# Optimization experiments

Measured on AMD Instinct MI355X. Metric: run time of the kernel, lower is better.

The kernel has to match this reference:

```python
import jax, jax.numpy as jnp
import numpy as np

B, T, N, D, H, M = 2, 12, 325, 64, 8, 3
EPS = 1e-6


def _layer_norm(x, g, b):
    mu = jnp.mean(x, axis=-1, keepdims=True)
    var = jnp.mean(jnp.square(x - mu), axis=-1, keepdims=True)
    return (x - mu) * jax.lax.rsqrt(var + EPS) * g + b


def _meta_w(ste, W1, b1, W2, b2):
    # ste: (b,t,n,d) -> per-token weight matrix (b,t,n,d,d)  [Meta_projection]
    h = jax.nn.relu(jnp.einsum('btnd,de->btne', ste, W1) + b1)
    w = jnp.einsum('btnd,df->btnf', h, W2) + b2
    b_, t_, n_, _ = ste.shape
    return w.reshape(b_, t_, n_, D, D)


def _meta_qkv(q, k, v, ste_q, ste_k, ste_v, mW1, mb1, mW2, mb2):
    wq = _meta_w(ste_q, mW1[0], mb1[0], mW2[0], mb2[0])
    wk = _meta_w(ste_k, mW1[1], mb1[1], mW2[1], mb2[1])
    wv = _meta_w(ste_v, mW1[2], mb1[2], mW2[2], mb2[2])
    mg = lambda x, w: jnp.einsum('btnd,btnde->btne', x, w)  # meta_guide
    return mg(q, wq), mg(k, wk), mg(v, wv)


def _split_heads(x):  # (B,L,d) -> (H*B,L,d/H), head-major = tf.concat(tf.split(x,H,-1),0)
    return jnp.concatenate(jnp.split(x, H, axis=-1), axis=0)


def _concat_heads(x):
    return jnp.concatenate(jnp.split(x, H, axis=0), axis=-1)


def _sdpa(q, k, v, tm=None):
    dk = q.shape[-1]
    scores = jnp.einsum('bqd,bkd->bqk', q, k) / jnp.sqrt(jnp.float32(dk))
    if tm is not None:  # spatial mask (n,n) broadcast over batch*heads
        scores = jnp.where(tm[None] > 0, scores, jnp.float32(-1e9))
    att = jax.nn.softmax(scores, axis=-1)
    return jnp.einsum('bqk,bkd->bqd', att, v)


def _temporal_attn(q, k, v, ste_q, ste_k, ste_v, mW1, mb1, mW2, mb2, Wo):
    b, t, n, d = q.shape
    qg, kg, vg = _meta_qkv(q, k, v, ste_q, ste_k, ste_v, mW1, mb1, mW2, mb2)
    rs = lambda x: x.transpose(0, 2, 1, 3).reshape(b * n, t, d)  # temporal_reshape
    out = _sdpa(_split_heads(rs(qg)), _split_heads(rs(kg)), _split_heads(rs(vg)))
    out = _concat_heads(out).reshape(b, n, t, d).transpose(0, 2, 1, 3)
    return jnp.einsum('btnd,de->btne', out, Wo)


def _spatial_attn(q, k, v, tms, ste_q, ste_k, ste_v, mW1, mb1, mW2, mb2, Wo):
    b, t, n, d = q.shape
    # meta weights are identical across the mask loop in the original -> compute once
    qg, kg, vg = _meta_qkv(q, k, v, ste_q, ste_k, ste_v, mW1, mb1, mW2, mb2)
    rs = lambda x: x.reshape(b * t, n, d)  # spatial_reshape
    q_, k_, v_ = _split_heads(rs(qg)), _split_heads(rs(kg)), _split_heads(rs(vg))
    m = tms.shape[0]
    outs = [_concat_heads(_sdpa(q_, k_, v_, tm=tms[i])) for i in range(m)]
    out = jnp.stack(outs).transpose(1, 2, 3, 0).reshape(b, t, n, d * m)
    return jnp.einsum('btnd,de->btne', out, Wo)


def _ffn(x, W1, W2):
    return jax.nn.relu(x @ W1) @ W2


def setup_inputs() -> dict:
    key = jax.random.key(0)
    ks = jax.random.split(key, 16)
    f = lambda i, shape, s=1.0: jax.random.normal(ks[i], shape, dtype=jnp.float32) * s
    return {
        'queries': f(0, (B, T, N, D)),
        'keys': f(1, (B, T, N, D)),
        'values': f(2, (B, T, N, D)),
        'ste_q': f(3, (B, T, N, D)),
        'ste_k': f(4, (B, T, N, D)),
        'ste_v': f(5, (B, T, N, D)),
        'tms': jax.random.randint(ks[6], (M, N, N), 0, 2, dtype=jnp.int32),
        # 4 attention modules (mta1, msa1, mta2, msa2), 3 meta branches each
        'mW1': f(7, (4, 3, D, D), 0.05),
        'mb1': jnp.zeros((4, 3, D), jnp.float32),
        'mW2': f(8, (4, 3, D, D * D), 0.02),
        'mb2': jnp.zeros((4, 3, D * D), jnp.float32),
        'Wo_t': f(9, (2, D, D), 0.05),          # temporal out-proj (no bias)
        'Wo_s': f(10, (2, M * D, D), 0.05),     # spatial out-proj over d*m (no bias)
        'ffn_W1': f(11, (2, D, D // 4), 0.05),
        'ffn_W2': f(12, (2, D // 4, D), 0.05),
        'ln_gamma': jnp.ones((6, D), jnp.float32),
        'ln_beta': jnp.zeros((6, D), jnp.float32),
    }


def reference(queries, keys, values, ste_q, ste_k, ste_v, tms,
              mW1, mb1, mW2, mb2, Wo_t, Wo_s, ffn_W1, ffn_W2, ln_gamma, ln_beta):
    # Encoderlayer with if_ste=True, if_meta=True, training=False (dropout = identity),
    # b_layers=m_layers=t_layers=1.
    tms_f = tms.astype(jnp.float32)
    x = queries
    # --- begin block: temporal attn + LN, spatial attn + LN ---
    out = _temporal_attn(x, keys, values, ste_q, ste_k, ste_v,
                         mW1[0], mb1[0], mW2[0], mb2[0], Wo_t[0])
    x = _layer_norm(x + out, ln_gamma[0], ln_beta[0])
    out = _spatial_attn(x, x, x, tms_f, ste_q, ste_k, ste_v,
                        mW1[1], mb1[1], mW2[1], mb2[1], Wo_s[0])
    x = _layer_norm(x + out, ln_gamma[1], ln_beta[1])
    # --- medium block: temporal + LN, spatial + LN, FFN + LN ---
    out = _temporal_attn(x, x, x, ste_q, ste_k, ste_v,
                         mW1[2], mb1[2], mW2[2], mb2[2], Wo_t[1])
    x = _layer_norm(x + out, ln_gamma[2], ln_beta[2])
    out = _spatial_attn(x, x, x, tms_f, ste_q, ste_k, ste_v,
                        mW1[3], mb1[3], mW2[3], mb2[3], Wo_s[1])
    x = _layer_norm(x + out, ln_gamma[3], ln_beta[3])
    out = _ffn(x, ffn_W1[0], ffn_W2[0])
    x = _layer_norm(x + out, ln_gamma[4], ln_beta[4])
    # --- end block: FFN + LN ---
    out = _ffn(x, ffn_W1[1], ffn_W2[1])
    x = _layer_norm(x + out, ln_gamma[5], ln_beta[5])
    return x
```

## Files before the change

### kernel.cpp

```cpp
#include <hip/hip_runtime.h>
#include <math.h>

#define BB 2
#define TT 12
#define NN 325
#define DD 64
#define HH 8
#define MM 3
#define NT (BB*TT*NN)
#define NT64 (NT*64)
#define EPS 1e-6f
#define KTOT 4160
#define SEGS 8
#define KPS 41
#define NR 328

typedef _Float16 f16x8 __attribute__((ext_vector_type(8)));
typedef _Float16 f16x2 __attribute__((ext_vector_type(2)));
typedef float f32x4 __attribute__((ext_vector_type(4)));
typedef float f32x2 __attribute__((ext_vector_type(2)));

#if __has_builtin(__builtin_amdgcn_exp2f)
#define EXP2F(x) __builtin_amdgcn_exp2f(x)
#else
#define EXP2F(x) exp2f(x)
#endif

__device__ inline float wave_reduce_sum(float v) {
    #pragma unroll
    for (int o = 32; o > 0; o >>= 1) v += __shfl_xor(v, o, 64);
    return v;
}

__global__ __launch_bounds__(256)
void wt_prep(const float* __restrict__ mW2, const float* __restrict__ mb2,
             _Float16* __restrict__ Wt) {
    const int p = blockIdx.y;
    const int kk0 = blockIdx.x * 64;
    __shared__ float s[64][65];
    const int tid = threadIdx.x;
    #pragma unroll
    for (int pass = 0; pass < 16; ++pass) {
        int idx = pass*256 + tid;
        int kl = idx >> 6, e = idx & 63;
        int kk = kk0 + kl;
        float v = (kk < 4096) ? mW2[(size_t)p*262144 + (size_t)kk*64 + e]
                              : mb2[(size_t)p*4096 + (size_t)(kk-4096)*64 + e];
        s[kl][e] = v;
    }
    __syncthreads();
    #pragma unroll
    for (int pass = 0; pass < 16; ++pass) {
        int idx = pass*256 + tid;
        int e = idx >> 6, kl = idx & 63;
        Wt[(size_t)p*64*KTOT + (size_t)e*KTOT + kk0 + kl] = (_Float16)s[kl][e];
    }
}

__global__ __launch_bounds__(256)
void prep2(const float* __restrict__ mW1, _Float16* __restrict__ W1f,
           const int* __restrict__ tms, unsigned* __restrict__ pmr) {
    const int tid = threadIdx.x;
    if (blockIdx.x < 12) {
        const int p = blockIdx.x;
        #pragma unroll
        for (int i = 0; i < 16; ++i) {
            int idx = i*256 + tid;
            int d = idx >> 6, e = idx & 63;
            W1f[(size_t)p*4096 + e*64 + d] = (_Float16)mW1[(size_t)p*4096 + d*64 + e];
        }
        return;
    }
    int idx = (blockIdx.x - 12)*256 + tid;
    if (idx >= MM*NN*SEGS) return;
    int seg = idx & 7;
    int nq = (idx >> 3) % NN;
    int i = idx / (SEGS*NN);
    int ks = seg*KPS;
    int ke = (ks + KPS < NN) ? ks + KPS : NN;
    const int* row = tms + ((size_t)i*NN + nq)*NN;
    unsigned w0 = 0, w1 = 0;
    for (int k = ks; k < ke; ++k) {
        int b = k - ks;
        unsigned bit = (row[k] > 0) ? 1u : 0u;
        if (b < 32) w0 |= bit << b; else w1 |= bit << (b - 32);
    }
    pmr[(size_t)idx*2]     = w0;
    pmr[(size_t)idx*2 + 1] = w1;
}

template<int MODE>
__global__ __launch_bounds__(256, 2)
void meta_gemm_t(const float* __restrict__ x0, const float* __restrict__ x1,
                 const float* __restrict__ x2,
                 const float* __restrict__ s0, const float* __restrict__ s1,
                 const float* __restrict__ s2,
                 const _Float16* __restrict__ W1f, const float* __restrict__ b1m,
                 const _Float16* __restrict__ Wtm,
                 void* __restrict__ o0, void* __restrict__ o1, void* __restrict__ o2) {
    const int br = blockIdx.y;
    const int t0 = blockIdx.x * 64;
    const float* xg = (br==0) ? x0 : (br==1) ? x1 : x2;
    const float* sg = (br==0) ? s0 : (br==1) ? s1 : s2;
    const _Float16* W1b = W1f + (size_t)br*4096;
    const float* b1g = b1m + (size_t)br*64;
    const _Float16* W = Wtm + (size_t)br*64*KTOT;
    void* outp = (br==0) ? o0 : (br==1) ? o1 : o2;

    __shared__ _Float16 sx[64*64];
    __shared__ _Float16 ss[64*64];
    __shared__ _Float16 shT[64*68];
    __shared__ _Float16 bB[2][1024*8];

    const int tid = threadIdx.x;
    #pragma unroll
    for (int i = 0; i < 2; ++i) {
        int idx = i*256 + tid;
        int row = idx >> 3, u = idx & 7;
        int t = t0 + row;
        int boff = row*128 + ((u*16) ^ ((row & 7) << 4));
        f16x8 xo, so;
        if (t < NT) {
            const float4* xp = (const float4*)(xg + (size_t)t*64 + u*8);
            float4 a = xp[0], b = xp[1];
            f16x8 xv = {(_Float16)a.x,(_Float16)a.y,(_Float16)a.z,(_Float16)a.w,
                        (_Float16)b.x,(_Float16)b.y,(_Float16)b.z,(_Float16)b.w};
            const float4* sp = (const float4*)(sg + (size_t)t*64 + u*8);
            float4 c = sp[0], d = sp[1];
            f16x8 sv = {(_Float16)c.x,(_Float16)c.y,(_Float16)c.z,(_Float16)c.w,
                        (_Float16)d.x,(_Float16)d.y,(_Float16)d.z,(_Float16)d.w};
            xo = xv; so = sv;
        } else {
            f16x8 z = {(_Float16)0.f,(_Float16)0.f,(_Float16)0.f,(_Float16)0.f,
                       (_Float16)0.f,(_Float16)0.f,(_Float16)0.f,(_Float16)0.f};
            xo = z; so = z;
        }
        *(f16x8*)((char*)sx + boff) = xo;
        *(f16x8*)((char*)ss + boff) = so;
    }
    __syncthreads();

    const int wid = tid >> 6, lane = tid & 63;
    const int col = lane & 15, g = lane >> 4;
    const int wm = wid & 1, wn = wid >> 1;
    const int trow0 = wm*32 + col;
    const int trow1 = trow0 + 16;
    const int rb0 = trow0*128, rb1 = trow1*128;
    const int sz = (trow0 & 7) << 4;

    {
        const int hrow = wid*16 + col;
        const int hrb = hrow*128;
        const int hsz = (hrow & 7) << 4;
        f32x4 ha[4] = {{0,0,0,0},{0,0,0,0},{0,0,0,0},{0,0,0,0}};
        #pragma unroll
        for (int ph = 0; ph < 2; ++ph) {
            int dd = ph*32 + g*8;
            f16x8 sv = *(f16x8*)((char*)ss + hrb + ((dd*2) ^ hsz));
            #pragma unroll
            for (int ni = 0; ni < 4; ++ni) {
                f16x8 bw = *(const f16x8*)(W1b + (size_t)(ni*16+col)*64 + dd);
                ha[ni] = __builtin_amdgcn_mfma_f32_16x16x32_f16(sv, bw, ha[ni], 0, 0, 0);
            }
        }
        #pragma unroll
        for (int ni = 0; ni < 4; ++ni) {
            float bv = b1g[ni*16+col];
            #pragma unroll
            for (int r = 0; r < 4; ++r)
                shT[(wid*16 + g*4 + r)*68 + ni*16 + col] = (_Float16)fmaxf(ha[ni][r] + bv, 0.f);
        }
    }

    f16x8 xv00 = *(f16x8*)((char*)sx + rb0 + (((g*8)*2) ^ sz));
    f16x8 xv01 = *(f16x8*)((char*)sx + rb0 + (((32 + g*8)*2) ^ sz));
    f16x8 xv10 = *(f16x8*)((char*)sx + rb1 + (((g*8)*2) ^ sz));
    f16x8 xv11 = *(f16x8*)((char*)sx + rb1 + (((32 + g*8)*2) ^ sz));

    auto STAGE2 = [&](int bi, int st2) {
        const _Float16* base = W + (size_t)st2*128;
        #pragma unroll
        for (int j = 0; j < 4; ++j) {
            int p = j*256 + tid;
            int t = p >> 9;
            int rest = p & 511;
            int e = rest >> 3, wu = rest & 7;
            const _Float16* src = base + (size_t)t*64 + (size_t)e*KTOT + ((wu ^ (e & 7)) << 3);
            __builtin_amdgcn_global_load_lds(
                (const __attribute__((address_space(1))) void*)src,
                (__attribute__((address_space(3))) void*)&bB[bi][p*8],
                16, 0, 0);
        }
    };
    auto STAGE1 = [&](int bi, int st) {
        const _Float16* base = W + (size_t)st*64;
        #pragma unroll
        for (int j = 0; j < 2; ++j) {
            int p = j*256 + tid;
            int e = p >> 3, wu = p & 7;
            const _Float16* src = base + (size_t)e*KTOT + ((wu ^ (e & 7)) << 3);
            __builtin_amdgcn_global_load_lds(
                (const __attribute__((address_space(1))) void*)src,
                (__attribute__((address_space(3))) void*)&bB[bi][p*8],
                16, 0, 0);
        }
    };

    STAGE2(0, 0);
    STAGE2(1, 1);
    asm volatile("s_waitcnt lgkmcnt(0)" ::: "memory");
    __builtin_amdgcn_sched_barrier(0);

    f32x4 A[2][2] = {{{0,0,0,0},{0,0,0,0}},{{0,0,0,0},{0,0,0,0}}};
    f16x8 hv0 = {}, hv1 = {};

    const int e0 = wn*32 + col;
    const int e1 = e0 + 16;
    const int u00 = e0*8 + (g ^ (e0 & 7));
    const int u01 = e0*8 + ((4 + g) ^ (e0 & 7));
    const int u10 = e1*8 + (g ^ (e1 & 7));
    const int u11 = e1*8 + ((4 + g) ^ (e1 & 7));

    auto COMPUTE = [&](const _Float16* Bb, int ci) {
        #pragma unroll
        for (int t = 0; t < 2; ++t) {
            _Float16 hc0 = hv0[ci*2 + t];
            _Float16 hc1 = hv1[ci*2 + t];
            const _Float16* Bs = Bb + t*512*8;
            f16x8 b00 = *(const f16x8*)((const char*)Bs + u00*16);
            f16x8 b01 = *(const f16x8*)((const char*)Bs + u01*16);
            f16x8 b10 = *(const f16x8*)((const char*)Bs + u10*16);
            f16x8 b11 = *(const f16x8*)((const char*)Bs + u11*16);
            f16x8 p00 = xv00 * hc0;
            f16x8 p10 = xv10 * hc1;
            A[0][0] = __builtin_amdgcn_mfma_f32_16x16x32_f16(p00, b00, A[0][0], 0, 0, 0);
            A[0][1] = __builtin_amdgcn_mfma_f32_16x16x32_f16(p00, b10, A[0][1], 0, 0, 0);
            A[1][0] = __builtin_amdgcn_mfma_f32_16x16x32_f16(p10, b00, A[1][0], 0, 0, 0);
            A[1][1] = __builtin_amdgcn_mfma_f32_16x16x32_f16(p10, b10, A[1][1], 0, 0, 0);
            f16x8 p01 = xv01 * hc0;
            f16x8 p11 = xv11 * hc1;
            A[0][0] = __builtin_amdgcn_mfma_f32_16x16x32_f16(p01, b01, A[0][0], 0, 0, 0);
            A[0][1] = __builtin_amdgcn_mfma_f32_16x16x32_f16(p01, b11, A[0][1], 0, 0, 0);
            A[1][0] = __builtin_amdgcn_mfma_f32_16x16x32_f16(p11, b01, A[1][0], 0, 0, 0);
            A[1][1] = __builtin_amdgcn_mfma_f32_16x16x32_f16(p11, b11, A[1][1], 0, 0, 0);
        }
    };

    for (int q = 0; q < 7; ++q) {
        #pragma unroll
        for (int s = 0; s < 4; ++s) {
            asm volatile("s_waitcnt vmcnt(4)" ::: "memory");
            __builtin_amdgcn_sched_barrier(0);
            __builtin_amdgcn_s_barrier();
            if (s == 0) {
                hv0 = *(f16x8*)&shT[trow0*68 + q*8];
                hv1 = *(f16x8*)&shT[trow1*68 + q*8];
            }
            COMPUTE(bB[s & 1], s);
            __builtin_amdgcn_s_barrier();
            STAGE2(s & 1, 4*q + s + 2);
        }
    }
    asm volatile("s_waitcnt vmcnt(4)" ::: "memory");
    __builtin_amdgcn_sched_barrier(0);
    __builtin_amdgcn_s_barrier();
    hv0 = *(f16x8*)&shT[trow0*68 + 56];
    hv1 = *(f16x8*)&shT[trow1*68 + 56];
    COMPUTE(bB[0], 0);
    __builtin_amdgcn_s_barrier();
    STAGE2(0, 30);

    asm volatile("s_waitcnt vmcnt(4)" ::: "memory");
    __builtin_amdgcn_sched_barrier(0);
    __builtin_amdgcn_s_barrier();
    COMPUTE(bB[1], 1);
    __builtin_amdgcn_s_barrier();
    STAGE2(1, 31);

    asm volatile("s_waitcnt vmcnt(4)" ::: "memory");
    __builtin_amdgcn_sched_barrier(0);
    __builtin_amdgcn_s_barrier();
    COMPUTE(bB[0], 2);
    __builtin_amdgcn_s_barrier();

    asm volatile("s_waitcnt vmcnt(0)" ::: "memory");
    __builtin_amdgcn_sched_barrier(0);
    __builtin_amdgcn_s_barrier();
    COMPUTE(bB[1], 3);
    __builtin_amdgcn_s_barrier();

    STAGE1(0, 64);
    asm volatile("s_waitcnt vmcnt(0)" ::: "memory");
    __builtin_amdgcn_sched_barrier(0);
    __builtin_amdgcn_s_barrier();
    {
        const _Float16* Bs = bB[0];
        f16x8 b00 = *(const f16x8*)((const char*)Bs + u00*16);
        f16x8 b01 = *(const f16x8*)((const char*)Bs + u01*16);
        f16x8 b10 = *(const f16x8*)((const char*)Bs + u10*16);
        f16x8 b11 = *(const f16x8*)((const char*)Bs + u11*16);
        A[0][0] = __builtin_amdgcn_mfma_f32_16x16x32_f16(xv00, b00, A[0][0], 0, 0, 0);
        A[0][1] = __builtin_amdgcn_mfma_f32_16x16x32_f16(xv00, b10, A[0][1], 0, 0, 0);
        A[1][0] = __builtin_amdgcn_mfma_f32_16x16x32_f16(xv10, b00, A[1][0], 0, 0, 0);
        A[1][1] = __builtin_amdgcn_mfma_f32_16x16x32_f16(xv10, b10, A[1][1], 0, 0, 0);
        A[0][0] = __builtin_amdgcn_mfma_f32_16x16x32_f16(xv01, b01, A[0][0], 0, 0, 0);
        A[0][1] = __builtin_amdgcn_mfma_f32_16x16x32_f16(xv01, b11, A[0][1], 0, 0, 0);
        A[1][0] = __builtin_amdgcn_mfma_f32_16x16x32_f16(xv11, b01, A[1][0], 0, 0, 0);
        A[1][1] = __builtin_amdgcn_mfma_f32_16x16x32_f16(xv11, b11, A[1][1], 0, 0, 0);
    }

    if (MODE == 0) {
        float* op = (float*)outp;
        #pragma unroll
        for (int mt = 0; mt < 2; ++mt) {
            #pragma unroll
            for (int nj = 0; nj < 2; ++nj) {
                const int e = e0 + nj*16;
                #pragma unroll
                for (int r = 0; r < 4; ++r) {
                    int t = t0 + wm*32 + mt*16 + g*4 + r;
                    if (t < NT) op[(size_t)t*64 + e] = A[mt][nj][r];
                }
            }
        }
    } else {
        const float KSC = 0.35355339059327373f * 1.4426950408889634f;
        const float scl = (br == 1) ? KSC : 1.f;
        const int bt0 = t0 / NN;
        const int bound = (bt0 + 1)*NN;
        _Float16* op = (_Float16*)outp;
        #pragma unroll
        for (int mt = 0; mt < 2; ++mt) {
            #pragma unroll
            for (int nj = 0; nj < 2; ++nj) {
                const int e = e0 + nj*16;
                const int hh = e >> 3, dd = e & 7;
                #pragma unroll
                for (int r = 0; r < 4; ++r) {
                    int t = t0 + wm*32 + mt*16 + g*4 + r;
                    if (t < NT) {
                        int bt = (t >= bound) ? bt0 + 1 : bt0;
                        int n = t - bt*NN;
                        size_t pidx = ((size_t)(bt*8 + hh)*NR + n)*8 + dd;
                        op[pidx] = (_Float16)(A[mt][nj][r]*scl);
                    }
                }
            }
        }
    }
}

__global__ __launch_bounds__(256)
void temporal_fused(const float* __restrict__ qg, const float* __restrict__ kg,
                    const float* __restrict__ vg, const float* __restrict__ xres,
                    const float* __restrict__ Wo, const float* __restrict__ gamma,
                    const float* __restrict__ beta, float* __restrict__ xout) {
    const int wid = threadIdx.x >> 6, lane = threadIdx.x & 63;
    const int token = blockIdx.x*4 + wid;
    if (token >= NT) return;
    const int n = token % NN;
    const int b = token / (NN*TT);
    const float scale = 0.35355339059327373f;
    const float qv = qg[(size_t)token*64 + lane] * scale;

    float s[TT], v[TT];
    #pragma unroll
    for (int kt = 0; kt < TT; ++kt) {
        size_t base = ((size_t)(b*TT + kt)*NN + n)*64 + lane;
        float kv = kg[base];
        v[kt] = vg[base];
        float d = qv * kv;
        d += __shfl_xor(d, 1, 64);
        d += __shfl_xor(d, 2, 64);
        d += __shfl_xor(d, 4, 64);
        s[kt] = d;
    }
    float m = s[0];
    #pragma unroll
    for (int kt = 1; kt < TT; ++kt) m = fmaxf(m, s[kt]);
    float l = 0.f, O = 0.f;
    #pragma unroll
    for (int kt = 0; kt < TT; ++kt) {
        float p = __expf(s[kt] - m);
        l += p;
        O += p * v[kt];
    }
    O /= l;
    float y = 0.f;
    #pragma unroll
    for (int d = 0; d < 64; ++d) y += __shfl(O, d, 64) * Wo[d*64 + lane];
    float r = xres[(size_t)token*64 + lane] + y;
    float mu = wave_reduce_sum(r) * (1.f/64.f);
    float diff = r - mu;
    float var = wave_reduce_sum(diff*diff) * (1.f/64.f);
    xout[(size_t)token*64 + lane] = diff * rsqrtf(var + EPS) * gamma[lane] + beta[lane];
}

__global__ __launch_bounds__(256)
void spatial_attn13(const _Float16* __restrict__ Qh, const _Float16* __restrict__ Kh,
                    const _Float16* __restrict__ Vh, const unsigned* __restrict__ pmr,
                    _Float16* __restrict__ outs) {
    const int bh = blockIdx.x;
    const int bt = bh >> 3, h = bh & 7;
    const int q0 = blockIdx.y * 32;
    __shared__ _Float16 KV[NR*16];
    const int tid = threadIdx.x;
    const _Float16* Kb = Kh + (size_t)bh*NR*8;
    const _Float16* Vb = Vh + (size_t)bh*NR*8;

    for (int u = tid; u < NR; u += 256) {
        *(f16x8*)&KV[u*16]     = *(const f16x8*)&Kb[u*8];
        *(f16x8*)&KV[u*16 + 8] = *(const f16x8*)&Vb[u*8];
    }
    __syncthreads();

    const int wid = tid >> 6, lane = tid & 63;
    const int qu = lane >> 3, seg = lane & 7;
    const int nq = q0 + wid*8 + qu;
    const bool act = nq < NN;
    const int qm = act ? nq : NN-1;

    f16x8 qv = *(const f16x8*)(Qh + ((size_t)bh*NR + qm)*8);
    const f16x2* qh2 = (const f16x2*)&qv;
    const int ks = seg*KPS;

    const size_t mbase = ((size_t)qm*SEGS + seg)*2;
    const size_t mstep = (size_t)NN*SEGS*2;
    unsigned w00 = pmr[mbase],           w01 = pmr[mbase+1];
    unsigned w10 = pmr[mstep+mbase],     w11 = pmr[mstep+mbase+1];
    unsigned w20 = pmr[2*mstep+mbase],   w21 = pmr[2*mstep+mbase+1];

    float l0 = 0.f, l1 = 0.f, l2 = 0.f;
    f32x2 O0[4] = {{0,0},{0,0},{0,0},{0,0}};
    f32x2 O1[4] = {{0,0},{0,0},{0,0},{0,0}};
    f32x2 O2[4] = {{0,0},{0,0},{0,0},{0,0}};

    f16x8 kc = *(const f16x8*)&KV[ks*16];
    f16x8 vc = *(const f16x8*)&KV[ks*16 + 8];

    auto step = [&](int j, unsigned b0, unsigned b1, unsigned b2) {
        f16x8 kn = kc, vn = vc;
        if (j + 1 < KPS) {
            kn = *(const f16x8*)&KV[(ks + j + 1)*16];
            vn = *(const f16x8*)&KV[(ks + j + 1)*16 + 8];
        }
        const f16x2* k2 = (const f16x2*)&kc;
        float d = __builtin_amdgcn_fdot2(qh2[0], k2[0], -32.f, false);
        d = __builtin_amdgcn_fdot2(qh2[1], k2[1], d, false);
        d = __builtin_amdgcn_fdot2(qh2[2], k2[2], d, false);
        d = __builtin_amdgcn_fdot2(qh2[3], k2[3], d, false);
        float E = EXP2F(d);
        float E0 = b0 ? E : 0.f;
        float E1 = b1 ? E : 0.f;
        float E2 = b2 ? E : 0.f;
        l0 += E0; l1 += E1; l2 += E2;
        f32x2 e0 = {E0, E0}, e1 = {E1, E1}, e2 = {E2, E2};
        #pragma unroll
        for (int jj = 0; jj < 4; ++jj) {
            f32x2 vp = {(float)vc[2*jj], (float)vc[2*jj+1]};
            O0[jj] += e0 * vp;
            O1[jj] += e1 * vp;
            O2[jj] += e2 * vp;
        }
        kc = kn; vc = vn;
    };
    #pragma unroll
    for (int j = 0; j < 32; ++j)
        step(j, (w00 >> j) & 1u, (w10 >> j) & 1u, (w20 >> j) & 1u);
    #pragma unroll
    for (int j = 32; j < KPS; ++j)
        step(j, (w01 >> (j-32)) & 1u, (w11 >> (j-32)) & 1u, (w21 >> (j-32)) & 1u);

    #pragma unroll
    for (int off = 1; off <= 4; off <<= 1) {
        l0 += __shfl_xor(l0, off, 64);
        l1 += __shfl_xor(l1, off, 64);
        l2 += __shfl_xor(l2, off, 64);
        #pragma unroll
        for (int j = 0; j < 4; ++j) {
            #pragma unroll
            for (int c = 0; c < 2; ++c) {
                O0[j][c] += __shfl_xor(O0[j][c], off, 64);
                O1[j][c] += __shfl_xor(O1[j][c], off, 64);
                O2[j][c] += __shfl_xor(O2[j][c], off, 64);
            }
        }
    }

    if (act && seg == 0) {
        float i0 = 1.f/l0, i1 = 1.f/l1, i2 = 1.f/l2;
        _Float16* op = outs + (size_t)(bt*NN + nq)*192 + h*8;
        f16x8 o0, o1, o2;
        #pragma unroll
        for (int j = 0; j < 4; ++j) {
            o0[2*j] = (_Float16)(O0[j][0]*i0); o0[2*j+1] = (_Float16)(O0[j][1]*i0);
            o1[2*j] = (_Float16)(O1[j][0]*i1); o1[2*j+1] = (_Float16)(O1[j][1]*i1);
            o2[2*j] = (_Float16)(O2[j][0]*i2); o2[2*j+1] = (_Float16)(O2[j][1]*i2);
        }
        *(f16x8*)(op)       = o0;
        *(f16x8*)(op + 64)  = o1;
        *(f16x8*)(op + 128) = o2;
    }
}

__global__ __launch_bounds__(256)
void proj_res_ln_s_kernel(const _Float16* __restrict__ a, const float* __restrict__ xres,
                          const float* __restrict__ Wo, const float* __restrict__ gamma,
                          const float* __restrict__ beta, float* __restrict__ xout) {
    const int wid = threadIdx.x >> 6, lane = threadIdx.x & 63;
    const int token = blockIdx.x*4 + wid;
    if (token >= NT) return;
    const _Float16* ap = a + (size_t)token*192;
    const float a0 = (float)ap[lane];
    const float a1 = (float)ap[64 + lane];
    const float a2 = (float)ap[128 + lane];
    float y = 0.f;
    #pragma unroll
    for (int d = 0; d < 64; ++d) {
        y += __shfl(a0, d, 64) * Wo[(d*3+0)*64 + lane];
        y += __shfl(a1, d, 64) * Wo[(d*3+1)*64 + lane];
        y += __shfl(a2, d, 64) * Wo[(d*3+2)*64 + lane];
    }
    float r = xres[(size_t)token*64 + lane] + y;
    float mu = wave_reduce_sum(r) * (1.f/64.f);
    float diff = r - mu;
    float var = wave_reduce_sum(diff*diff) * (1.f/64.f);
    xout[(size_t)token*64 + lane] = diff * rsqrtf(var + EPS) * gamma[lane] + beta[lane];
}

__global__ __launch_bounds__(256)
void tail_fused(const _Float16* __restrict__ a, const float* __restrict__ xres,
                const float* __restrict__ Wo,
                const float* __restrict__ W1a, const float* __restrict__ W2a,
                const float* __restrict__ W1b, const float* __restrict__ W2b,
                const float* __restrict__ ln_g, const float* __restrict__ ln_b,
                float* __restrict__ out) {
    const int wid = threadIdx.x >> 6, lane = threadIdx.x & 63;
    const int token = blockIdx.x*4 + wid;
    if (token >= NT) return;
    const int c = lane & 15;

    const _Float16* ap = a + (size_t)token*192;
    const float a0 = (float)ap[lane];
    const float a1 = (float)ap[64 + lane];
    const float a2 = (float)ap[128 + lane];
    float y = 0.f;
    #pragma unroll
    for (int d = 0; d < 64; ++d) {
        y += __shfl(a0, d, 64) * Wo[(d*3+0)*64 + lane];
        y += __shfl(a1, d, 64) * Wo[(d*3+1)*64 + lane];
        y += __shfl(a2, d, 64) * Wo[(d*3+2)*64 + lane];
    }
    float r = xres[(size_t)token*64 + lane] + y;
    float mu = wave_reduce_sum(r) * (1.f/64.f);
    float diff = r - mu;
    float var = wave_reduce_sum(diff*diff) * (1.f/64.f);
    float x1 = diff * rsqrtf(var + EPS) * ln_g[lane] + ln_b[lane];

    float hs = 0.f;
    #pragma unroll
    for (int d = 0; d < 64; ++d) hs += __shfl(x1, d, 64) * W1a[d*16 + c];
    float hr = fmaxf(hs, 0.f);
    float y2 = 0.f;
    #pragma unroll
    for (int cc = 0; cc < 16; ++cc) y2 += __shfl(hr, cc, 64) * W2a[cc*64 + lane];
    r = x1 + y2;
    mu = wave_reduce_sum(r) * (1.f/64.f);
    diff = r - mu;
    var = wave_reduce_sum(diff*diff) * (1.f/64.f);
    float x2 = diff * rsqrtf(var + EPS) * ln_g[64 + lane] + ln_b[64 + lane];

    hs = 0.f;
    #pragma unroll
    for (int d = 0; d < 64; ++d) hs += __shfl(x2, d, 64) * W1b[d*16 + c];
    hr = fmaxf(hs, 0.f);
    y2 = 0.f;
    #pragma unroll
    for (int cc = 0; cc < 16; ++cc) y2 += __shfl(hr, cc, 64) * W2b[cc*64 + lane];
    r = x2 + y2;
    mu = wave_reduce_sum(r) * (1.f/64.f);
    diff = r - mu;
    var = wave_reduce_sum(diff*diff) * (1.f/64.f);
    out[(size_t)token*64 + lane] = diff * rsqrtf(var + EPS) * ln_g[128 + lane] + ln_b[128 + lane];
}

extern "C" void kernel_launch(void* const* d_in, const int* in_sizes, int n_in,
                              void* d_out, int out_size, void* d_ws, size_t ws_size,
                              hipStream_t stream) {
    const float* queries = (const float*)d_in[0];
    const float* keys    = (const float*)d_in[1];
    const float* values  = (const float*)d_in[2];
    const float* ste_q   = (const float*)d_in[3];
    const float* ste_k   = (const float*)d_in[4];
    const float* ste_v   = (const float*)d_in[5];
    const int*   tms     = (const int*)d_in[6];
    const float* mW1     = (const float*)d_in[7];
    const float* mb1     = (const float*)d_in[8];
    const float* mW2     = (const float*)d_in[9];
    const float* mb2     = (const float*)d_in[10];
    const float* Wo_t    = (const float*)d_in[11];
    const float* Wo_s    = (const float*)d_in[12];
    const float* ffn_W1  = (const float*)d_in[13];
    const float* ffn_W2  = (const float*)d_in[14];
    const float* ln_g    = (const float*)d_in[15];
    const float* ln_b    = (const float*)d_in[16];

    char* p = (char*)d_ws;
    auto carve = [&](size_t bytes) { char* r = p; p += (bytes + 255) & ~(size_t)255; return r; };
    float* xbuf = (float*)carve((size_t)NT64*4);
    float* qg   = (float*)carve((size_t)NT64*4);
    float* kg   = (float*)carve((size_t)NT64*4);
    float* vg   = (float*)carve((size_t)NT64*4);
    _Float16* as_ = (_Float16*)carve((size_t)NT*192*2);
    _Float16* Wt  = (_Float16*)carve((size_t)12*64*KTOT*2);
    _Float16* W1f = (_Float16*)carve((size_t)12*4096*2);
    unsigned* pmr = (unsigned*)carve((size_t)MM*NN*SEGS*2*4);
    _Float16* Qh  = (_Float16*)carve((size_t)BB*TT*HH*NR*8*2);
    _Float16* Kh  = (_Float16*)carve((size_t)BB*TT*HH*NR*8*2);
    _Float16* Vh  = (_Float16*)carve((size_t)BB*TT*HH*NR*8*2);

    const dim3 blk(256);
    const dim3 g_tok(NT/4);
    const dim3 g_sa(BB*TT*HH, 11);
    const dim3 g_gemm((NT + 63)/64, 3);

    wt_prep<<<dim3(KTOT/64, 12), blk, 0, stream>>>(mW2, mb2, Wt);
    prep2<<<dim3(12 + (MM*NN*SEGS + 255)/256), blk, 0, stream>>>(mW1, W1f, tms, pmr);

    meta_gemm_t<0><<<g_gemm, blk, 0, stream>>>(
        queries, keys, values, ste_q, ste_k, ste_v,
        W1f, mb1, Wt, (void*)qg, (void*)kg, (void*)vg);
    temporal_fused<<<g_tok, blk, 0, stream>>>(
        qg, kg, vg, queries, Wo_t, ln_g, ln_b, xbuf);

    meta_gemm_t<1><<<g_gemm, blk, 0, stream>>>(
        xbuf, xbuf, xbuf, ste_q, ste_k, ste_v,
        W1f + (size_t)3*4096, mb1 + (size_t)3*64, Wt + (size_t)3*64*KTOT,
        (void*)Qh, (void*)Kh, (void*)Vh);
    spatial_attn13<<<g_sa, blk, 0, stream>>>(Qh, Kh, Vh, pmr, as_);
    proj_res_ln_s_kernel<<<g_tok, blk, 0, stream>>>(
        as_, xbuf, Wo_s, ln_g + 64, ln_b + 64, xbuf);

    meta_gemm_t<0><<<g_gemm, blk, 0, stream>>>(
        xbuf, xbuf, xbuf, ste_q, ste_k, ste_v,
        W1f + (size_t)6*4096, mb1 + (size_t)6*64, Wt + (size_t)6*64*KTOT,
        (void*)qg, (void*)kg, (void*)vg);
    temporal_fused<<<g_tok, blk, 0, stream>>>(
        qg, kg, vg, xbuf, Wo_t + (size_t)64*64, ln_g + 128, ln_b + 128, xbuf);

    meta_gemm_t<1><<<g_gemm, blk, 0, stream>>>(
        xbuf, xbuf, xbuf, ste_q, ste_k, ste_v,
        W1f + (size_t)9*4096, mb1 + (size_t)9*64, Wt + (size_t)9*64*KTOT,
        (void*)Qh, (void*)Kh, (void*)Vh);
    spatial_attn13<<<g_sa, blk, 0, stream>>>(Qh, Kh, Vh, pmr, as_);
    tail_fused<<<g_tok, blk, 0, stream>>>(
        as_, xbuf, Wo_s + (size_t)192*64,
        ffn_W1, ffn_W2, ffn_W1 + (size_t)64*16, ffn_W2 + (size_t)16*64,
        ln_g + 192, ln_b + 192, (float*)d_out);
}
```

Baseline: 247.5 us.

## Deepen meta GEMM weight pipeline to four LDS slots with aliased buffers

```diff
diff --git a/kernel.cpp b/kernel.cpp
--- a/kernel.cpp
+++ b/kernel.cpp
@@ -107,12 +107,46 @@
     const _Float16* W = Wtm + (size_t)br*64*KTOT;
     void* outp = (br==0) ? o0 : (br==1) ? o1 : o2;
 
-    __shared__ _Float16 sx[64*64];
-    __shared__ _Float16 ss[64*64];
-    __shared__ _Float16 shT[64*68];
-    __shared__ _Float16 bB[2][1024*8];
+    __shared__ __align__(16) char smem[74240];
+    _Float16* sx  = (_Float16*)(smem);
+    _Float16* ss  = (_Float16*)(smem + 8192);
+    _Float16* shT = (_Float16*)(smem + 16384);
+    _Float16* const slot0 = (_Float16*)(smem + 25088);
+    _Float16* const slot1 = (_Float16*)(smem + 41472);
+    _Float16* const slot2 = (_Float16*)(smem);
+    _Float16* const slot3 = (_Float16*)(smem + 57856);
 
     const int tid = threadIdx.x;
+
+    auto STAGE2 = [&](_Float16* dst, int st2) {
+        const _Float16* base = W + (size_t)st2*128;
+        #pragma unroll
+        for (int j = 0; j < 4; ++j) {
+            int p = j*256 + tid;
+            int t = p >> 9;
+            int rest = p & 511;
+            int e = rest >> 3, wu = rest & 7;
+            const _Float16* src = base + (size_t)t*64 + (size_t)e*KTOT + ((wu ^ (e & 7)) << 3);
+            __builtin_amdgcn_global_load_lds(
+                (const __attribute__((address_space(1))) void*)src,
+                (__attribute__((address_space(3))) void*)&dst[p*8],
+                16, 0, 0);
+        }
+    };
+    auto STAGE1 = [&](_Float16* dst, int st) {
+        const _Float16* base = W + (size_t)st*64;
+        #pragma unroll
+        for (int j = 0; j < 2; ++j) {
+            int p = j*256 + tid;
+            int e = p >> 3, wu = p & 7;
+            const _Float16* src = base + (size_t)e*KTOT + ((wu ^ (e & 7)) << 3);
+            __builtin_amdgcn_global_load_lds(
+                (const __attribute__((address_space(1))) void*)src,
+                (__attribute__((address_space(3))) void*)&dst[p*8],
+                16, 0, 0);
+        }
+    };
+
     #pragma unroll
     for (int i = 0; i < 2; ++i) {
         int idx = i*256 + tid;
@@ -138,7 +172,13 @@
         *(f16x8*)((char*)sx + boff) = xo;
         *(f16x8*)((char*)ss + boff) = so;
     }
-    __syncthreads();
+
+    STAGE2(slot0, 0);
+    STAGE2(slot1, 1);
+
+    asm volatile("s_waitcnt lgkmcnt(0)" ::: "memory");
+    __builtin_amdgcn_sched_barrier(0);
+    __builtin_amdgcn_s_barrier();
 
     const int wid = tid >> 6, lane = tid & 63;
     const int col = lane & 15, g = lane >> 4;
@@ -177,39 +217,12 @@
     f16x8 xv10 = *(f16x8*)((char*)sx + rb1 + (((g*8)*2) ^ sz));
     f16x8 xv11 = *(f16x8*)((char*)sx + rb1 + (((32 + g*8)*2) ^ sz));
 
-    auto STAGE2 = [&](int bi, int st2) {
-        const _Float16* base = W + (size_t)st2*128;
-        #pragma unroll
-        for (int j = 0; j < 4; ++j) {
-            int p = j*256 + tid;
-            int t = p >> 9;
-            int rest = p & 511;
-            int e = rest >> 3, wu = rest & 7;
-            const _Float16* src = base + (size_t)t*64 + (size_t)e*KTOT + ((wu ^ (e & 7)) << 3);
-            __builtin_amdgcn_global_load_lds(
-                (const __attribute__((address_space(1))) void*)src,
-                (__attribute__((address_space(3))) void*)&bB[bi][p*8],
-                16, 0, 0);
-        }
-    };
-    auto STAGE1 = [&](int bi, int st) {
-        const _Float16* base = W + (size_t)st*64;
-        #pragma unroll
-        for (int j = 0; j < 2; ++j) {
-            int p = j*256 + tid;
-            int e = p >> 3, wu = p & 7;
-            const _Float16* src = base + (size_t)e*KTOT + ((wu ^ (e & 7)) << 3);
-            __builtin_amdgcn_global_load_lds(
-                (const __attribute__((address_space(1))) void*)src,
-                (__attribute__((address_space(3))) void*)&bB[bi][p*8],
-                16, 0, 0);
-        }
-    };
-
-    STAGE2(0, 0);
-    STAGE2(1, 1);
     asm volatile("s_waitcnt lgkmcnt(0)" ::: "memory");
     __builtin_amdgcn_sched_barrier(0);
+    __builtin_amdgcn_s_barrier();
+
+    STAGE2(slot2, 2);
+    STAGE2(slot3, 3);
 
     f32x4 A[2][2] = {{{0,0,0,0},{0,0,0,0}},{{0,0,0,0},{0,0,0,0}}};
     f16x8 hv0 = {}, hv1 = {};
@@ -249,52 +262,51 @@
     for (int q = 0; q < 7; ++q) {
         #pragma unroll
         for (int s = 0; s < 4; ++s) {
-            asm volatile("s_waitcnt vmcnt(4)" ::: "memory");
+            asm volatile("s_waitcnt vmcnt(12)" ::: "memory");
             __builtin_amdgcn_sched_barrier(0);
             __builtin_amdgcn_s_barrier();
             if (s == 0) {
                 hv0 = *(f16x8*)&shT[trow0*68 + q*8];
                 hv1 = *(f16x8*)&shT[trow1*68 + q*8];
             }
-            COMPUTE(bB[s & 1], s);
+            _Float16* const sp = (s==0) ? slot0 : (s==1) ? slot1 : (s==2) ? slot2 : slot3;
+            COMPUTE(sp, s);
             __builtin_amdgcn_s_barrier();
-            STAGE2(s & 1, 4*q + s + 2);
-        }
-    }
-    asm volatile("s_waitcnt vmcnt(4)" ::: "memory");
+            STAGE2(sp, 4*q + s + 4);
+        }
+    }
+    asm volatile("s_waitcnt vmcnt(12)" ::: "memory");
     __builtin_amdgcn_sched_barrier(0);
     __builtin_amdgcn_s_barrier();
     hv0 = *(f16x8*)&shT[trow0*68 + 56];
     hv1 = *(f16x8*)&shT[trow1*68 + 56];
-    COMPUTE(bB[0], 0);
-    __builtin_amdgcn_s_barrier();
-    STAGE2(0, 30);
-
-    asm volatile("s_waitcnt vmcnt(4)" ::: "memory");
+    COMPUTE(slot0, 0);
+    __builtin_amdgcn_s_barrier();
+    STAGE1(slot0, 64);
+
+    asm volatile("s_waitcnt vmcnt(10)" ::: "memory");
     __builtin_amdgcn_sched_barrier(0);
     __builtin_amdgcn_s_barrier();
-    COMPUTE(bB[1], 1);
-    __builtin_amdgcn_s_barrier();
-    STAGE2(1, 31);
-
-    asm volatile("s_waitcnt vmcnt(4)" ::: "memory");
+    COMPUTE(slot1, 1);
+    __builtin_amdgcn_s_barrier();
+
+    asm volatile("s_waitcnt vmcnt(6)" ::: "memory");
     __builtin_amdgcn_sched_barrier(0);
     __builtin_amdgcn_s_barrier();
-    COMPUTE(bB[0], 2);
+    COMPUTE(slot2, 2);
+    __builtin_amdgcn_s_barrier();
+
+    asm volatile("s_waitcnt vmcnt(2)" ::: "memory");
+    __builtin_amdgcn_sched_barrier(0);
+    __builtin_amdgcn_s_barrier();
+    COMPUTE(slot3, 3);
     __builtin_amdgcn_s_barrier();
 
     asm volatile("s_waitcnt vmcnt(0)" ::: "memory");
     __builtin_amdgcn_sched_barrier(0);
     __builtin_amdgcn_s_barrier();
-    COMPUTE(bB[1], 3);
-    __builtin_amdgcn_s_barrier();
-
-    STAGE1(0, 64);
-    asm volatile("s_waitcnt vmcnt(0)" ::: "memory");
-    __builtin_amdgcn_sched_barrier(0);
-    __builtin_amdgcn_s_barrier();
     {
-        const _Float16* Bs = bB[0];
+        const _Float16* Bs = slot0;
         f16x8 b00 = *(const f16x8*)((const char*)Bs + u00*16);
         f16x8 b01 = *(const f16x8*)((const char*)Bs + u01*16);
         f16x8 b10 = *(const f16x8*)((const char*)Bs + u10*16);
```

After: 257.5 us. 4.0% more time.
